# Kernel tuning notes

Hardware: AMD Instinct MI355X
Metric: run time of the kernel (lower is better)

The kernel has to match this reference:

```python
import jax, jax.numpy as jnp
import numpy as np

# PercentClosenessBoosting (not in provided source): standard form is
#   new_boost = boost_tensor + (1 - tensor / tensor.max()) * boost_percent
# i.e. units far from the max get boosted more.

def _fwd_math(x, boost_tensor, sparsity, boost_percent):
    B, E = x.shape
    # --- run_boosting ---
    new_boost = boost_tensor + (1.0 - x / jnp.max(x)) * boost_percent
    boosted = jnp.maximum(x, 0.0) + new_boost
    # inhibition tensor starts empty -> apply_sparse_self_affector is a no-op
    # --- run_k_winners_positive: top-k (max_active) per row of boosted, binarize ---
    order = jnp.argsort(-boosted, axis=1)          # descending sort indices
    rank = jnp.argsort(order, axis=1)              # rank of each element in its row
    max_active = jnp.ceil(sparsity[1] * E)
    saved = jnp.where((rank < max_active) & (boosted > 0), 1.0, 0.0)  # ctx.save_for_backward
    # --- choose_boosted_to_satisfy_minimum (note: GLOBAL sum vs per-row min, faithful) ---
    min_active = jnp.floor(sparsity[0] * E)
    active = jnp.sum(saved)
    to_activate = jnp.ceil(min_active - active)
    border = jnp.argsort(-new_boost, axis=1)
    brank = jnp.argsort(border, axis=1)
    need = active < min_active
    out = jnp.where(need & (brank < to_activate), 1.0, saved)
    # --- zero boost where active ---
    final_boost = jnp.where(out > 0, jnp.zeros_like(new_boost), new_boost)
    return out, final_boost, saved


def setup_inputs() -> dict:
    key = jax.random.key(0)
    k1, = jax.random.split(key, 1)
    B, E = 64, 131072
    x = jax.random.normal(k1, (B, E), dtype=jnp.float32)
    boost_tensor = jnp.zeros((B, E), dtype=jnp.float32)
    sparsity = jnp.array([0.002, 0.02], dtype=jnp.float32)
    boost_percent = jnp.float32(1e-8)
    return {"x": x, "boost_tensor": boost_tensor, "sparsity": sparsity, "boost_percent": boost_percent}


def reference(x, boost_tensor, sparsity, boost_percent):
    out, final_boost, _ = _fwd_math(x, boost_tensor, sparsity, boost_percent)
    return out, final_boost
```

## Files before the change

### kernel.cpp

```cpp
#include <hip/hip_runtime.h>

#define BR 64
#define EC 131072
#define CAP 8192
#define LCAP 1024
#define CHUNKS 16
#define CHUNK_V (EC / CHUNKS / 4)
#define NSCH 41
#define NS (NSCH * 64)
#define SSTRIDE 3197
#define BINS 4096
#define BD 512

typedef float nf4 __attribute__((ext_vector_type(4)));

#define WS_GMAX 0
#define WS_CCNT 264
#define WS_NPOS 640
#define WS_BMAX 1024
#define CAND_U_OFF 4096
#define CAND_I_OFF (CAND_U_OFF + BR * CAP)

__device__ __forceinline__ unsigned map_f(float f) {
    unsigned b = __float_as_uint(f);
    return (b & 0x80000000u) ? ~b : (b | 0x80000000u);
}
__device__ __forceinline__ float unmap_f(unsigned u) {
    unsigned b = (u & 0x80000000u) ? (u & 0x7FFFFFFFu) : ~u;
    return __uint_as_float(b);
}

__device__ __forceinline__ void compute_vals(float x, float bt, float gmax, float bp,
                                             float* nb, float* bo) {
#pragma clang fp contract(off)
    float q = x / gmax;
    float t = 1.0f - q;
    float p = t * bp;
    float nbv = bt + p;
    *nb = nbv;
    *bo = fmaxf(x, 0.0f) + nbv;
}

__device__ __forceinline__ unsigned umax_(unsigned a, unsigned b) { return a > b ? a : b; }
__device__ __forceinline__ unsigned umin_(unsigned a, unsigned b) { return a < b ? a : b; }

__device__ __forceinline__ unsigned calc_K(const float* sp) {
    unsigned K = (unsigned)ceilf(sp[1] * (float)EC);
    if (K > EC) K = EC;
    if (K == 0) K = 1;
    return K;
}

__device__ unsigned lds_radix_select(const unsigned* su, unsigned n, unsigned K,
                                     unsigned* hist, unsigned* scan, unsigned* sb,
                                     int t, unsigned* krem) {
    unsigned pv = 0, Kp = K;
    for (int pass = 0; pass < 4; ++pass) {
        int shift = 24 - 8 * pass;
        hist[t] = 0;
        __syncthreads();
        for (unsigned i = t; i < n; i += 256) {
            unsigned u = su[i];
            bool match = (pass == 0) || ((u >> (shift + 8)) == (pv >> (shift + 8)));
            if (match) atomicAdd(&hist[(u >> shift) & 0xFFu], 1u);
        }
        __syncthreads();
        unsigned my = hist[t];
        scan[t] = my;
        __syncthreads();
        for (int off = 1; off < 256; off <<= 1) {
            unsigned v = (t + off < 256) ? scan[t + off] : 0u;
            __syncthreads();
            scan[t] += v;
            __syncthreads();
        }
        unsigned incl = scan[t], excl = incl - my;
        if (excl < Kp && incl >= Kp) {
            sb[0] = pv | ((unsigned)t << shift);
            sb[1] = Kp - excl;
        }
        __syncthreads();
        pv = sb[0];
        Kp = sb[1];
        __syncthreads();
    }
    *krem = Kp;
    return pv;
}

template<int USE_NB>
__device__ unsigned row_select_full(const float* xr, const float* br, float gmax,
                                    float bp, unsigned K, unsigned* hist,
                                    unsigned* aux, int t, unsigned* cut_out) {
    unsigned prefix = 0, Kp = K;
    for (int pass = 0; pass < 4; ++pass) {
        int shift = 24 - 8 * pass;
        hist[t] = 0;
        __syncthreads();
        for (int i = t; i < EC; i += 256) {
            float nb, bo;
            compute_vals(xr[i], br[i], gmax, bp, &nb, &bo);
            unsigned u = map_f(USE_NB ? nb : bo);
            bool match = (pass == 0) || ((u >> (shift + 8)) == (prefix >> (shift + 8)));
            if (match) atomicAdd(&hist[(u >> shift) & 0xFFu], 1u);
        }
        __syncthreads();
        if (t == 0) {
            unsigned cum = 0, bsel = 0, kr = Kp;
            for (int b = 255; b >= 0; --b) {
                unsigned h = hist[b];
                if (cum + h >= Kp) { bsel = (unsigned)b; kr = Kp - cum; break; }
                cum += h;
            }
            aux[0] = prefix | (bsel << shift);
            aux[1] = kr;
        }
        __syncthreads();
        prefix = aux[0];
        Kp = aux[1];
        __syncthreads();
    }
    unsigned u_t = prefix, ties = Kp;
    if (t == 0) { aux[6] = 0; aux[7] = 0xFFFFFFFFu; }
    __syncthreads();
    int wid = t >> 6, lane = t & 63;
    for (int base0 = 0; base0 < EC; base0 += 256) {
        int i = base0 + t;
        float nb, bo;
        compute_vals(xr[i], br[i], gmax, bp, &nb, &bo);
        bool eq = (map_f(USE_NB ? nb : bo) == u_t);
        unsigned long long bal = __ballot(eq);
        if (lane == 0) aux[2 + wid] = (unsigned)__popcll(bal);
        __syncthreads();
        unsigned run = aux[6];
        unsigned wpre = 0;
        for (int w = 0; w < wid; ++w) wpre += aux[2 + w];
        if (eq) {
            unsigned r = run + wpre + (unsigned)__popcll(bal & ((1ull << lane) - 1ull));
            if (r == ties - 1) aux[7] = (unsigned)i;
        }
        __syncthreads();
        if (t == 0) aux[6] = run + aux[2] + aux[3] + aux[4] + aux[5];
        __syncthreads();
        if (aux[6] >= ties) break;
    }
    if (t == 0) *cut_out = aux[7];
    __syncthreads();
    return u_t;
}

__global__ __launch_bounds__(256) void kA(const float4* __restrict__ x4,
                                          unsigned* __restrict__ ws) {
    if (blockIdx.x == 0)
        for (int i = threadIdx.x; i < 1024; i += 256) ws[i] = 0u;
    unsigned m = 0;
    const int nvec = BR * EC / 4;
    int stride = gridDim.x * 256;
    for (int v = blockIdx.x * 256 + threadIdx.x; v < nvec; v += stride) {
        float4 xv = x4[v];
        m = umax_(m, map_f(xv.x)); m = umax_(m, map_f(xv.y));
        m = umax_(m, map_f(xv.z)); m = umax_(m, map_f(xv.w));
    }
    for (int off = 32; off; off >>= 1) m = umax_(m, __shfl_down(m, off, 64));
    __shared__ unsigned sm[4];
    if ((threadIdx.x & 63) == 0) sm[threadIdx.x >> 6] = m;
    __syncthreads();
    if (threadIdx.x == 0)
        ws[WS_BMAX + blockIdx.x] = umax_(umax_(sm[0], sm[1]), umax_(sm[2], sm[3]));
}

__global__ __launch_bounds__(BD) void kB(const float* __restrict__ x,
                                         const float* __restrict__ bt,
                                         const float* __restrict__ sp,
                                         const float* __restrict__ bp_p,
                                         unsigned* __restrict__ ws,
                                         nf4* __restrict__ out4,
                                         nf4* __restrict__ fb4) {
    __shared__ unsigned hist[BINS];
    __shared__ unsigned lu[LCAP], li[LCAP];
    __shared__ unsigned ssum[256], sabove[256];
    __shared__ unsigned sred[8];
    __shared__ unsigned stlo, slcnt, sgbase;
    int t = threadIdx.x;
    int lane = t & 63;
    int row = blockIdx.x >> 4, chunk = blockIdx.x & (CHUNKS - 1);

    unsigned m = 0;
    for (int i = t; i < 1024; i += BD) m = umax_(m, ws[WS_BMAX + i]);
    for (int off = 32; off; off >>= 1) m = umax_(m, __shfl_down(m, off, 64));
    if (lane == 0) sred[t >> 6] = m;
    __syncthreads();
    unsigned gmu = 0;
    #pragma unroll
    for (int w = 0; w < BD / 64; ++w) gmu = umax_(gmu, sred[w]);
    if (blockIdx.x == 0 && t == 0) ws[WS_GMAX] = gmu;
    float gmax = unmap_f(gmu);
    float bp = *bp_p;

    for (int i = t; i < BINS; i += BD) hist[i] = 0;
    if (t == 0) slcnt = 0;
    __syncthreads();
    const float* xr = x + (size_t)row * EC;
    const float* br = bt + (size_t)row * EC;
    for (int s = t; s < NS; s += BD) {
        int idx = (s >> 6) * SSTRIDE + (s & 63);
        float nb, bo;
        compute_vals(xr[idx], br[idx], gmax, bp, &nb, &bo);
        atomicAdd(&hist[map_f(bo) >> 20], 1u);
    }
    __syncthreads();

    unsigned K = calc_K(sp);
    unsigned R = (unsigned)ceilf(1.75f * (float)NS * (float)K / (float)EC);
    if (R < 32) R = 32;
    if (R > NS) R = NS;
    if (t < 256) {
        unsigned hv[16];
        unsigned s = 0;
        #pragma unroll
        for (int j = 0; j < 16; ++j) { hv[j] = hist[t * 16 + j]; s += hv[j]; }
        ssum[t] = s;
        __syncthreads();
        if (t == 0) {
            unsigned acc = 0;
            for (int q = 255; q >= 0; --q) { sabove[q] = acc; acc += ssum[q]; }
        }
        __syncthreads();
        unsigned cum = sabove[t];
        for (int j = 15; j >= 0; --j) {
            unsigned h = hv[j];
            if (cum < R && cum + h >= R) stlo = ((unsigned)(t * 16 + j)) << 20;
            cum += h;
        }
    } else {
        __syncthreads();
        __syncthreads();
    }
    __syncthreads();
    unsigned tlo = stlo ? stlo - 1u : 0u;

    const float4* x4 = (const float4*)x;
    const float4* bt4 = (const float4*)bt;
    unsigned* cu = ws + CAND_U_OFF + (size_t)row * CAP;
    unsigned* ci = ws + CAND_I_OFF + (size_t)row * CAP;
    size_t base = (size_t)row * (EC / 4) + (size_t)chunk * CHUNK_V;
    int ebase = chunk * (EC / CHUNKS);
    const nf4 zo = {0.0f, 0.0f, 0.0f, 0.0f};
    unsigned posc = 0;
    for (int v = t; v < CHUNK_V; v += BD) {
        float4 xv = x4[base + v];
        float4 bv = bt4[base + v];
        float xs[4] = {xv.x, xv.y, xv.z, xv.w};
        float bs[4] = {bv.x, bv.y, bv.z, bv.w};
        nf4 fv;
        unsigned uj[4];
        #pragma unroll
        for (int j = 0; j < 4; ++j) {
            float nb, bo;
            compute_vals(xs[j], bs[j], gmax, bp, &nb, &bo);
            uj[j] = map_f(bo);
            fv[j] = nb;
            posc += (uj[j] > 0x80000000u) ? 1u : 0u;
        }
        __builtin_nontemporal_store(zo, &out4[base + v]);
        __builtin_nontemporal_store(fv, &fb4[base + v]);
        #pragma unroll
        for (int j = 0; j < 4; ++j) {
            bool match = (uj[j] > tlo);
            unsigned long long bal = __ballot(match);
            if (bal) {
                int leader = (int)(__ffsll((long long)bal) - 1);
                unsigned cnt = (unsigned)__popcll(bal);
                unsigned b0 = 0;
                if (lane == leader) b0 = atomicAdd(&slcnt, cnt);
                unsigned wbase = __shfl(b0, leader, 64);
                if (match) {
                    unsigned p = wbase + (unsigned)__popcll(bal & ((1ull << lane) - 1ull));
                    unsigned idx = (unsigned)(ebase + v * 4 + j);
                    if (p < LCAP) {
                        lu[p] = uj[j]; li[p] = idx;
                    } else {
                        unsigned gp = atomicAdd(&ws[WS_CCNT + row], 1u);
                        if (gp < CAP) { cu[gp] = uj[j]; ci[gp] = idx; }
                    }
                }
            }
        }
    }
    for (int off = 32; off; off >>= 1) posc += __shfl_down(posc, off, 64);
    if (lane == 0) sred[t >> 6] = posc;
    __syncthreads();
    if (t == 0) {
        unsigned tot = 0;
        #pragma unroll
        for (int w = 0; w < BD / 64; ++w) tot += sred[w];
        atomicAdd(&ws[WS_NPOS + row], tot);
    }
    __syncthreads();
    unsigned n = slcnt < LCAP ? slcnt : LCAP;
    if (t == 0) sgbase = atomicAdd(&ws[WS_CCNT + row], n);
    __syncthreads();
    unsigned gb = sgbase;
    for (unsigned i = t; i < n; i += BD) {
        unsigned gp = gb + i;
        if (gp < CAP) { cu[gp] = lu[i]; ci[gp] = li[i]; }
    }
}

__global__ __launch_bounds__(256) void kC(const float* __restrict__ x,
                                          const float* __restrict__ bt,
                                          const float* __restrict__ sp,
                                          const float* __restrict__ bp_p,
                                          unsigned* __restrict__ ws,
                                          float* __restrict__ out,
                                          float* __restrict__ fb) {
    int row = blockIdx.x;
    int t = threadIdx.x;
    unsigned n = ws[WS_CCNT + row];
    unsigned K = calc_K(sp);
    float gmax = unmap_f(ws[WS_GMAX]);
    float bp = *bp_p;
    const float* xr = x + (size_t)row * EC;
    const float* br = bt + (size_t)row * EC;
    float* outr = out + (size_t)row * EC;
    float* fbr = fb + (size_t)row * EC;
    __shared__ unsigned su[CAP];
    __shared__ unsigned hist[256], scan[256], sb[2];
    __shared__ unsigned marr[256];
    __shared__ unsigned mcnt;
    __shared__ unsigned aux[8];
    __shared__ unsigned sact, scut;
    if (n >= K && n <= CAP) {
        const unsigned* cu = ws + CAND_U_OFF + (size_t)row * CAP;
        const unsigned* ci = ws + CAND_I_OFF + (size_t)row * CAP;
        for (unsigned i = t; i < n; i += 256) su[i] = cu[i];
        if (t == 0) mcnt = 0;
        __syncthreads();
        unsigned krem2;
        unsigned u_t = lds_radix_select(su, n, K, hist, scan, sb, t, &krem2);
        for (unsigned i = t; i < n; i += 256)
            if (su[i] == u_t) {
                unsigned p = atomicAdd(&mcnt, 1u);
                if (p < 256) marr[p] = ci[i];
            }
        __syncthreads();
        unsigned m = mcnt;
        if (m <= 256) {
            for (unsigned i = t; i < m; i += 256) {
                unsigned myidx = marr[i];
                unsigned r = 0;
                for (unsigned j = 0; j < m; ++j) r += (marr[j] < myidx) ? 1u : 0u;
                if (r == krem2 - 1) scut = myidx;
            }
        } else {
            for (unsigned i = t; i < n; i += 256) {
                if (su[i] == u_t) {
                    unsigned myidx = ci[i];
                    unsigned r = 0;
                    for (unsigned j = 0; j < n; ++j)
                        if (su[j] == u_t && ci[j] < myidx) ++r;
                    if (r == krem2 - 1) scut = myidx;
                }
            }
        }
        __syncthreads();
        unsigned cut = scut;
        for (unsigned i = t; i < n; i += 256) {
            unsigned u = su[i], idx = ci[i];
            bool sel = (u > u_t) || ((u == u_t) && (idx <= cut));
            if (sel && u > 0x80000000u) { outr[idx] = 1.0f; fbr[idx] = 0.0f; }
        }
    } else {
        unsigned u_t = row_select_full<0>(xr, br, gmax, bp, K, hist, aux, t, &scut);
        unsigned cut = scut;
        for (int i = t; i < EC; i += 256) {
            float nb, bo;
            compute_vals(xr[i], br[i], gmax, bp, &nb, &bo);
            unsigned u = map_f(bo);
            bool sel = (u > u_t) || ((u == u_t) && ((unsigned)i <= cut));
            if (sel && u > 0x80000000u) { outr[i] = 1.0f; fbr[i] = 0.0f; }
        }
    }

    unsigned act = 0;
    if (t < 64) act = umin_(K, ws[WS_NPOS + t]);
    for (int off = 32; off; off >>= 1) act += __shfl_down(act, off, 64);
    if (t == 0) sact = act;
    __syncthreads();
    float active = (float)sact;
    float min_active = floorf(sp[0] * (float)EC);
    if (active < min_active) {
        unsigned K2 = (unsigned)ceilf(min_active - active);
        if (K2 > EC) K2 = EC;
        unsigned ut2 = row_select_full<1>(xr, br, gmax, bp, K2, hist, aux, t, &scut);
        unsigned cut2 = scut;
        for (int i = t; i < EC; i += 256) {
            float nb, bo;
            compute_vals(xr[i], br[i], gmax, bp, &nb, &bo);
            unsigned u2 = map_f(nb);
            if (u2 > ut2 || (u2 == ut2 && (unsigned)i <= cut2)) {
                outr[i] = 1.0f;
                fbr[i] = 0.0f;
            }
        }
    }
}

extern "C" void kernel_launch(void* const* d_in, const int* in_sizes, int n_in,
                              void* d_out, int out_size, void* d_ws, size_t ws_size,
                              hipStream_t stream) {
    const float* x  = (const float*)d_in[0];
    const float* bt = (const float*)d_in[1];
    const float* sp = (const float*)d_in[2];
    const float* bp = (const float*)d_in[3];
    float* out = (float*)d_out;
    float* fb  = out + (size_t)BR * EC;
    unsigned* ws = (unsigned*)d_ws;

    kA<<<1024, 256, 0, stream>>>((const float4*)x, ws);
    kB<<<BR * CHUNKS, BD, 0, stream>>>(x, bt, sp, bp, ws, (nf4*)out, (nf4*)fb);
    kC<<<BR, 256, 0, stream>>>(x, bt, sp, bp, ws, out, fb);
}
```

Measured before the change: 73.73 us.

## Move per-row threshold histogram from kB into kA and enlarge candidate cap

The per-row sampled histogram and threshold search move out of each of the 16 chunk blocks per row in kB and into the first 64 blocks of kA, which store one threshold per row in the workspace. The histogram now uses an approximation of boosted (relu(x)+boost_tensor, ignoring the tiny boost term), and the threshold sits one bin lower to leave slack, so CAP grows to hold more candidates. kB also stops using nontemporal stores and fully unrolls compute_vals. The intent is to drop redundant histogram work and shared memory from kB. In exchange kA gains a serial tail on 64 blocks, and more candidates may overflow into global memory.

```diff
diff --git a/kernel.cpp b/kernel.cpp
--- a/kernel.cpp
+++ b/kernel.cpp
@@ -2,7 +2,7 @@
 
 #define BR 64
 #define EC 131072
-#define CAP 8192
+#define CAP 12288
 #define LCAP 1024
 #define CHUNKS 16
 #define CHUNK_V (EC / CHUNKS / 4)
@@ -18,6 +18,7 @@
 #define WS_CCNT 264
 #define WS_NPOS 640
 #define WS_BMAX 1024
+#define WS_TLO 2048
 #define CAND_U_OFF 4096
 #define CAND_I_OFF (CAND_U_OFF + BR * CAP)
 
@@ -149,38 +150,82 @@
     return u_t;
 }
 
-__global__ __launch_bounds__(256) void kA(const float4* __restrict__ x4,
+__global__ __launch_bounds__(256) void kA(const float* __restrict__ x,
+                                          const float* __restrict__ bt,
+                                          const float* __restrict__ sp,
                                           unsigned* __restrict__ ws) {
+    __shared__ unsigned hist[BINS];
+    __shared__ unsigned ssum[256], sabove[256];
+    __shared__ unsigned sm[4];
+    __shared__ unsigned sb1;
+    int t = threadIdx.x;
     if (blockIdx.x == 0)
-        for (int i = threadIdx.x; i < 1024; i += 256) ws[i] = 0u;
+        for (int i = t; i < 1024; i += 256) ws[i] = 0u;
+    const float4* x4 = (const float4*)x;
     unsigned m = 0;
     const int nvec = BR * EC / 4;
     int stride = gridDim.x * 256;
-    for (int v = blockIdx.x * 256 + threadIdx.x; v < nvec; v += stride) {
+    for (int v = blockIdx.x * 256 + t; v < nvec; v += stride) {
         float4 xv = x4[v];
         m = umax_(m, map_f(xv.x)); m = umax_(m, map_f(xv.y));
         m = umax_(m, map_f(xv.z)); m = umax_(m, map_f(xv.w));
     }
     for (int off = 32; off; off >>= 1) m = umax_(m, __shfl_down(m, off, 64));
-    __shared__ unsigned sm[4];
-    if ((threadIdx.x & 63) == 0) sm[threadIdx.x >> 6] = m;
-    __syncthreads();
-    if (threadIdx.x == 0)
+    if ((t & 63) == 0) sm[t >> 6] = m;
+    __syncthreads();
+    if (t == 0)
         ws[WS_BMAX + blockIdx.x] = umax_(umax_(sm[0], sm[1]), umax_(sm[2], sm[3]));
+
+    if (blockIdx.x >= BR) return;
+    int row = blockIdx.x;
+    for (int i = t; i < BINS; i += 256) hist[i] = 0;
+    if (t == 0) sb1 = 0;
+    __syncthreads();
+    const float* xr = x + (size_t)row * EC;
+    const float* br = bt + (size_t)row * EC;
+    for (int s = t; s < NS; s += 256) {
+        int idx = (s >> 6) * SSTRIDE + (s & 63);
+        float sv = fmaxf(xr[idx], 0.0f) + br[idx];
+        atomicAdd(&hist[map_f(sv) >> 20], 1u);
+    }
+    __syncthreads();
+    unsigned K = calc_K(sp);
+    unsigned R = (unsigned)ceilf(1.75f * (float)NS * (float)K / (float)EC);
+    if (R < 32) R = 32;
+    if (R > NS) R = NS;
+    unsigned hv[16];
+    unsigned s = 0;
+    #pragma unroll
+    for (int j = 0; j < 16; ++j) { hv[j] = hist[t * 16 + j]; s += hv[j]; }
+    ssum[t] = s;
+    __syncthreads();
+    if (t == 0) {
+        unsigned acc = 0;
+        for (int q = 255; q >= 0; --q) { sabove[q] = acc; acc += ssum[q]; }
+    }
+    __syncthreads();
+    unsigned cum = sabove[t];
+    for (int j = 15; j >= 0; --j) {
+        unsigned h = hv[j];
+        if (cum < R && cum + h >= R) sb1 = (unsigned)(t * 16 + j);
+        cum += h;
+    }
+    __syncthreads();
+    if (t == 0) {
+        unsigned b1 = sb1;
+        ws[WS_TLO + row] = (b1 >= 1) ? (((b1 - 1) << 20) - 1u) : 0u;
+    }
 }
 
 __global__ __launch_bounds__(BD) void kB(const float* __restrict__ x,
                                          const float* __restrict__ bt,
-                                         const float* __restrict__ sp,
                                          const float* __restrict__ bp_p,
                                          unsigned* __restrict__ ws,
-                                         nf4* __restrict__ out4,
-                                         nf4* __restrict__ fb4) {
-    __shared__ unsigned hist[BINS];
+                                         float4* __restrict__ out4,
+                                         float4* __restrict__ fb4) {
     __shared__ unsigned lu[LCAP], li[LCAP];
-    __shared__ unsigned ssum[256], sabove[256];
     __shared__ unsigned sred[8];
-    __shared__ unsigned stlo, slcnt, sgbase;
+    __shared__ unsigned slcnt, sgbase;
     int t = threadIdx.x;
     int lane = t & 63;
     int row = blockIdx.x >> 4, chunk = blockIdx.x & (CHUNKS - 1);
@@ -189,6 +234,7 @@
     for (int i = t; i < 1024; i += BD) m = umax_(m, ws[WS_BMAX + i]);
     for (int off = 32; off; off >>= 1) m = umax_(m, __shfl_down(m, off, 64));
     if (lane == 0) sred[t >> 6] = m;
+    if (t == 0) slcnt = 0;
     __syncthreads();
     unsigned gmu = 0;
     #pragma unroll
@@ -196,48 +242,7 @@
     if (blockIdx.x == 0 && t == 0) ws[WS_GMAX] = gmu;
     float gmax = unmap_f(gmu);
     float bp = *bp_p;
-
-    for (int i = t; i < BINS; i += BD) hist[i] = 0;
-    if (t == 0) slcnt = 0;
-    __syncthreads();
-    const float* xr = x + (size_t)row * EC;
-    const float* br = bt + (size_t)row * EC;
-    for (int s = t; s < NS; s += BD) {
-        int idx = (s >> 6) * SSTRIDE + (s & 63);
-        float nb, bo;
-        compute_vals(xr[idx], br[idx], gmax, bp, &nb, &bo);
-        atomicAdd(&hist[map_f(bo) >> 20], 1u);
-    }
-    __syncthreads();
-
-    unsigned K = calc_K(sp);
-    unsigned R = (unsigned)ceilf(1.75f * (float)NS * (float)K / (float)EC);
-    if (R < 32) R = 32;
-    if (R > NS) R = NS;
-    if (t < 256) {
-        unsigned hv[16];
-        unsigned s = 0;
-        #pragma unroll
-        for (int j = 0; j < 16; ++j) { hv[j] = hist[t * 16 + j]; s += hv[j]; }
-        ssum[t] = s;
-        __syncthreads();
-        if (t == 0) {
-            unsigned acc = 0;
-            for (int q = 255; q >= 0; --q) { sabove[q] = acc; acc += ssum[q]; }
-        }
-        __syncthreads();
-        unsigned cum = sabove[t];
-        for (int j = 15; j >= 0; --j) {
-            unsigned h = hv[j];
-            if (cum < R && cum + h >= R) stlo = ((unsigned)(t * 16 + j)) << 20;
-            cum += h;
-        }
-    } else {
-        __syncthreads();
-        __syncthreads();
-    }
-    __syncthreads();
-    unsigned tlo = stlo ? stlo - 1u : 0u;
+    unsigned tlo = ws[WS_TLO + row];
 
     const float4* x4 = (const float4*)x;
     const float4* bt4 = (const float4*)bt;
@@ -245,25 +250,25 @@
     unsigned* ci = ws + CAND_I_OFF + (size_t)row * CAP;
     size_t base = (size_t)row * (EC / 4) + (size_t)chunk * CHUNK_V;
     int ebase = chunk * (EC / CHUNKS);
-    const nf4 zo = {0.0f, 0.0f, 0.0f, 0.0f};
+    const float4 zo = make_float4(0.0f, 0.0f, 0.0f, 0.0f);
     unsigned posc = 0;
     for (int v = t; v < CHUNK_V; v += BD) {
         float4 xv = x4[base + v];
         float4 bv = bt4[base + v];
         float xs[4] = {xv.x, xv.y, xv.z, xv.w};
         float bs[4] = {bv.x, bv.y, bv.z, bv.w};
-        nf4 fv;
+        float4 fv;
         unsigned uj[4];
+        float nb0, nb1, nb2, nb3, bo_;
+        compute_vals(xs[0], bs[0], gmax, bp, &nb0, &bo_); uj[0] = map_f(bo_);
+        compute_vals(xs[1], bs[1], gmax, bp, &nb1, &bo_); uj[1] = map_f(bo_);
+        compute_vals(xs[2], bs[2], gmax, bp, &nb2, &bo_); uj[2] = map_f(bo_);
+        compute_vals(xs[3], bs[3], gmax, bp, &nb3, &bo_); uj[3] = map_f(bo_);
+        fv = make_float4(nb0, nb1, nb2, nb3);
         #pragma unroll
-        for (int j = 0; j < 4; ++j) {
-            float nb, bo;
-            compute_vals(xs[j], bs[j], gmax, bp, &nb, &bo);
-            uj[j] = map_f(bo);
-            fv[j] = nb;
-            posc += (uj[j] > 0x80000000u) ? 1u : 0u;
-        }
-        __builtin_nontemporal_store(zo, &out4[base + v]);
-        __builtin_nontemporal_store(fv, &fb4[base + v]);
+        for (int j = 0; j < 4; ++j) posc += (uj[j] > 0x80000000u) ? 1u : 0u;
+        out4[base + v] = zo;
+        fb4[base + v] = fv;
         #pragma unroll
         for (int j = 0; j < 4; ++j) {
             bool match = (uj[j] > tlo);
@@ -417,7 +422,7 @@
     float* fb  = out + (size_t)BR * EC;
     unsigned* ws = (unsigned*)d_ws;
 
-    kA<<<1024, 256, 0, stream>>>((const float4*)x, ws);
-    kB<<<BR * CHUNKS, BD, 0, stream>>>(x, bt, sp, bp, ws, (nf4*)out, (nf4*)fb);
+    kA<<<1024, 256, 0, stream>>>(x, bt, sp, ws);
+    kB<<<BR * CHUNKS, BD, 0, stream>>>(x, bt, bp, ws, (float4*)out, (float4*)fb);
     kC<<<BR, 256, 0, stream>>>(x, bt, sp, bp, ws, out, fb);
 }
```

Measured after the change: 77.27 us. +4.8%, slower.
